# Kernel optimization log

Hardware: AMD Instinct MI355X
Metric: run time of the kernel (lower is better)

The kernel has to match this reference:

```python
import jax, jax.numpy as jnp
import numpy as np


def mlp(x, W1, b1, W2, b2):
    # x: [D] -> y: [O]
    return jnp.tanh(x @ W1 + b1) @ W2 + b2


def christoffel(x, W1, b1, W2, b2):
    """Per-example Christoffel symbols Gamma[k,i,j] for one point x: [D].

    Faithful to the torch code: the 'metric' used for Gamma is built from
    gradients of the FIRST n_dims outputs (y_flat[:, i], i < n_dims), i.e.
    G = Jn Jn^T with Jn the jacobian restricted to the first D outputs.
    """
    D = x.shape[-1]
    f = lambda z: mlp(z, W1, b1, W2, b2)[:D]          # first D outputs

    def metric(z):
        J = jax.jacrev(f)(z)                           # [D, D]
        return J @ J.T                                 # G[i,j] = grad_i . grad_j

    dG = jax.jacfwd(metric)(x)                         # dG[i,j,k] = dG_ij/dx_k
    # Gamma[k,i,j] = 0.5 * (dG[i,j,k] + dG[i,k,j] - dG[j,k,i])
    return 0.5 * (dG.transpose((2, 0, 1)) + dG.transpose((1, 0, 2)) - dG.transpose((1, 2, 0)))


def setup_inputs() -> dict:
    key = jax.random.key(0)
    k1, k2, k3, k4, k5 = jax.random.split(key, 5)
    B, D, H, O = 32, 64, 2048, 64
    return {
        "x0": jnp.zeros((B, D), jnp.float32),
        "xT": jax.random.normal(k1, (B, D), jnp.float32),
        "W1": jax.random.normal(k2, (D, H), jnp.float32) / np.sqrt(D),
        "b1": jax.random.normal(k3, (H,), jnp.float32) * 0.02,
        "W2": jax.random.normal(k4, (H, O), jnp.float32) / np.sqrt(H),
        "b2": jax.random.normal(k5, (O,), jnp.float32) * 0.02,
        "n_steps": 10,
    }


def reference(x0, xT, W1, b1, W2, b2, n_steps):
    B, D = x0.shape
    t = jnp.linspace(0.0, 1.0, n_steps)                    # [S]
    # straight-line interpolation paths  [S, B, D]
    straight = x0[None] + t[:, None, None] * (xT - x0)[None]
    v = xT - x0
    v = v / jnp.linalg.norm(v, axis=1, keepdims=True)      # [B, D]

    interior = straight[1:-1].reshape(-1, D)               # [(S-2)*B, D]
    Gamma = jax.vmap(christoffel, in_axes=(0, None, None, None, None))(
        interior, W1, b1, W2, b2
    ).reshape(n_steps - 2, B, D, D, D)                     # [S-2, B, k, i, j]

    # correction[b,mu] = -sum_{k,i} Gamma[b,k,i,mu] v[b,k] v[b,i]
    corr = -jnp.einsum('sbkim,bk,bi->sbm', Gamma, v, v)    # [S-2, B, D]
    t_int = t[1:-1]
    t_factor = (t_int * (1.0 - t_int))[:, None, None]
    scale = jnp.minimum(jnp.linalg.norm(corr, axis=2, keepdims=True), 0.1)
    corr = corr * t_factor * scale * 0.1

    paths = straight.at[1:-1].add(corr)                    # [S, B, D]
    return paths.reshape(-1, D)                            # [S*B, D]
```

## Files before the change

kernel.cpp:

```cpp
#include <hip/hip_runtime.h>
#include <math.h>


#define D64 64

__device__ __forceinline__ unsigned short f2bf(float x) {
    unsigned u = __float_as_uint(x);
    u += 0x7FFFu + ((u >> 16) & 1u);
    return (unsigned short)(u >> 16);
}
__device__ __forceinline__ float bf_lo(unsigned u) { return __uint_as_float(u << 16); }
__device__ __forceinline__ float bf_hi(unsigned u) { return __uint_as_float(u & 0xFFFF0000u); }

__global__ __launch_bounds__(256) void k_prep(
    const float* __restrict__ x0, const float* __restrict__ xT,
    const float* __restrict__ W1, const float* __restrict__ b1,
    const float* __restrict__ W2,
    unsigned short* __restrict__ W1b,
    float* __restrict__ Z0, float* __restrict__ Zd, float* __restrict__ C,
    float* __restrict__ out, int B, int H, int n_steps)
{
    const int b   = blockIdx.y;
    const int tid = threadIdx.x;
    const int h   = blockIdx.x * 256 + tid;

    __shared__ float x0L[D64], dL[D64], vL[D64];
    if (tid < D64) {
        const float a0 = x0[b * D64 + tid];
        const float aT = xT[b * D64 + tid];
        const float d  = aT - a0;
        float ss = d * d;
        #pragma unroll
        for (int off = 32; off; off >>= 1) ss += __shfl_xor(ss, off);
        const float inv = 1.0f / sqrtf(ss);
        x0L[tid] = a0; dL[tid] = d; vL[tid] = d * inv;
        if (blockIdx.x == 0) {
            out[(size_t)(0 * B + b) * D64 + tid]             = a0;
            out[(size_t)((n_steps - 1) * B + b) * D64 + tid] = aT;
        }
    }
    __syncthreads();

    float z0 = b1[h];
    float zd = 0.f;
    if (b == 0) {
        #pragma unroll
        for (int d = 0; d < D64; ++d) {
            const float w = W1[(size_t)d * H + h];
            W1b[(size_t)d * H + h] = f2bf(w);
            z0 = fmaf(x0L[d], w, z0);
            zd = fmaf(dL[d],  w, zd);
        }
    } else {
        #pragma unroll
        for (int d = 0; d < D64; ++d) {
            const float w = W1[(size_t)d * H + h];
            z0 = fmaf(x0L[d], w, z0);
            zd = fmaf(dL[d],  w, zd);
        }
    }

    float c = 0.f;
    const float4* w2r = reinterpret_cast<const float4*>(W2 + (size_t)h * D64);
    #pragma unroll
    for (int i = 0; i < D64 / 4; ++i) {
        const float4 w = w2r[i];
        c = fmaf(w.x, vL[4*i],     c);
        c = fmaf(w.y, vL[4*i + 1], c);
        c = fmaf(w.z, vL[4*i + 2], c);
        c = fmaf(w.w, vL[4*i + 3], c);
    }

    Z0[(size_t)b * H + h] = z0;
    Zd[(size_t)b * H + h] = zd;
    C [(size_t)b * H + h] = c;
}

__global__ __launch_bounds__(1024) void k_fused(
    const float* __restrict__ x0, const float* __restrict__ xT,
    const unsigned short* __restrict__ W1b,
    const float* __restrict__ Z0, const float* __restrict__ Zd,
    const float* __restrict__ C,
    float* __restrict__ out, int B, int H, int n_steps)
{
    const int n    = blockIdx.x;
    const int s8   = n / B;
    const int b    = n % B;
    const int tid  = threadIdx.x;
    const int lane = tid & 63;
    const int wv   = tid >> 6;

    __shared__ float pL[2048];
    __shared__ float qL[2048];
    __shared__ float gradL[D64];
    __shared__ float corrL[D64];

    const float ts = (float)(s8 + 1) / (float)(n_steps - 1);

    {
        const float2 z0 = reinterpret_cast<const float2*>(Z0 + (size_t)b * H)[tid];
        const float2 zd = reinterpret_cast<const float2*>(Zd + (size_t)b * H)[tid];
        const float2 c  = reinterpret_cast<const float2*>(C  + (size_t)b * H)[tid];
        const float zx = fmaf(ts, zd.x, z0.x);
        const float zy = fmaf(ts, zd.y, z0.y);
        const float tx = tanhf(zx), ty = tanhf(zy);
        const float sx = 1.f - tx * tx, sy = 1.f - ty * ty;
        pL[2 * tid]     = c.x * sx;
        pL[2 * tid + 1] = c.y * sy;
        qL[2 * tid]     = -2.f * c.x * tx * sx;
        qL[2 * tid + 1] = -2.f * c.y * ty * sy;
    }
    __syncthreads();

    #pragma unroll
    for (int rr = 0; rr < 4; ++rr) {
        const int a = wv * 4 + rr;
        const uint4* wrow = reinterpret_cast<const uint4*>(W1b + (size_t)a * H);
        float acc = 0.f;
        #pragma unroll
        for (int k = 0; k < 4; ++k) {
            const uint4  w  = wrow[lane + k * 64];
            const float4 p0 = reinterpret_cast<const float4*>(pL)[(lane + k * 64) * 2];
            const float4 p1 = reinterpret_cast<const float4*>(pL)[(lane + k * 64) * 2 + 1];
            acc = fmaf(bf_lo(w.x), p0.x, acc);
            acc = fmaf(bf_hi(w.x), p0.y, acc);
            acc = fmaf(bf_lo(w.y), p0.z, acc);
            acc = fmaf(bf_hi(w.y), p0.w, acc);
            acc = fmaf(bf_lo(w.z), p1.x, acc);
            acc = fmaf(bf_hi(w.z), p1.y, acc);
            acc = fmaf(bf_lo(w.w), p1.z, acc);
            acc = fmaf(bf_hi(w.w), p1.w, acc);
        }
        #pragma unroll
        for (int off = 32; off; off >>= 1) acc += __shfl_xor(acc, off);
        if (lane == 0) gradL[a] = acc;
    }
    __syncthreads();

    {
        float2 r = make_float2(0.f, 0.f);
        #pragma unroll 16
        for (int d = 0; d < D64; ++d) {
            const unsigned w = reinterpret_cast<const unsigned*>(W1b + (size_t)d * H)[tid];
            const float    g = gradL[d];
            r.x = fmaf(g, bf_lo(w), r.x);
            r.y = fmaf(g, bf_hi(w), r.y);
        }
        pL[2 * tid]     = qL[2 * tid]     * r.x;
        pL[2 * tid + 1] = qL[2 * tid + 1] * r.y;
    }
    __syncthreads();

    #pragma unroll
    for (int rr = 0; rr < 4; ++rr) {
        const int a = wv * 4 + rr;
        const uint4* wrow = reinterpret_cast<const uint4*>(W1b + (size_t)a * H);
        float acc = 0.f;
        #pragma unroll
        for (int k = 0; k < 4; ++k) {
            const uint4  w  = wrow[lane + k * 64];
            const float4 p0 = reinterpret_cast<const float4*>(pL)[(lane + k * 64) * 2];
            const float4 p1 = reinterpret_cast<const float4*>(pL)[(lane + k * 64) * 2 + 1];
            acc = fmaf(bf_lo(w.x), p0.x, acc);
            acc = fmaf(bf_hi(w.x), p0.y, acc);
            acc = fmaf(bf_lo(w.y), p0.z, acc);
            acc = fmaf(bf_hi(w.y), p0.w, acc);
            acc = fmaf(bf_lo(w.z), p1.x, acc);
            acc = fmaf(bf_hi(w.z), p1.y, acc);
            acc = fmaf(bf_lo(w.w), p1.z, acc);
            acc = fmaf(bf_hi(w.w), p1.w, acc);
        }
        #pragma unroll
        for (int off = 32; off; off >>= 1) acc += __shfl_xor(acc, off);
        if (lane == 0) corrL[a] = -acc;
    }
    __syncthreads();

    if (tid < D64) {
        const float a0 = x0[b * D64 + tid];
        const float aT = xT[b * D64 + tid];
        const float d  = aT - a0;
        const float cm = corrL[tid];
        float n2 = cm * cm;
        #pragma unroll
        for (int off = 32; off; off >>= 1) n2 += __shfl_xor(n2, off);
        const float scale  = fminf(sqrtf(n2), 0.1f);
        const float factor = ts * (1.f - ts) * scale * 0.1f;
        out[(size_t)((s8 + 1) * B + b) * D64 + tid] = fmaf(cm, factor, fmaf(ts, d, a0));
    }
}

extern "C" void kernel_launch(void* const* d_in, const int* in_sizes, int n_in,
                              void* d_out, int out_size, void* d_ws, size_t ws_size,
                              hipStream_t stream) {
    const float* x0 = (const float*)d_in[0];
    const float* xT = (const float*)d_in[1];
    const float* W1 = (const float*)d_in[2];
    const float* b1 = (const float*)d_in[3];
    const float* W2 = (const float*)d_in[4];
    float* out = (float*)d_out;

    const int H       = in_sizes[3];
    const int D       = in_sizes[2] / H;
    const int B       = in_sizes[0] / D;
    const int n_steps = out_size / (B * D);
    const int NI      = n_steps - 2;
    const int NP      = NI * B;

    unsigned short* W1b = (unsigned short*)d_ws;
    float* Z0 = (float*)(W1b + (size_t)D * H);
    float* Zd = Z0 + (size_t)B * H;
    float* C  = Zd + (size_t)B * H;

    k_prep<<<dim3(H / 256, B), dim3(256), 0, stream>>>(
        x0, xT, W1, b1, W2, W1b, Z0, Zd, C, out, B, H, n_steps);
    k_fused<<<dim3(NP), dim3(1024), 0, stream>>>(
        x0, xT, W1b, Z0, Zd, C, out, B, H, n_steps);
}
```

Measured before the change: 81.64 us.

## Merge prep and fused kernels into one cooperative kernel with grid sync

Replaces the two-kernel sequence with a single cooperative launch of NP blocks. Each block first computes a 256-wide chunk of Z0/Zd/C, splitting the D reduction across four thread groups and combining the partials in shared memory, and converts a slice of W1 to bf16. A grid-wide sync follows, then the per-point fused Gamma contraction runs as before. This removes a kernel launch boundary and redistributes the prep work over more threads, at the cost of a grid barrier and of requiring all 256 blocks of 1024 threads to be co-resident. The chunk mapping relies on NP*512 equalling D*H and on NI being H/256, which matches only these shapes.

After: 123.7 us. 51.5% more time.

```diff
diff --git a/kernel.cpp b/kernel.cpp
--- a/kernel.cpp
+++ b/kernel.cpp
@@ -1,8 +1,12 @@
 #include <hip/hip_runtime.h>
+#include <hip/hip_cooperative_groups.h>
 #include <math.h>
 
+namespace cg = cooperative_groups;
+
 
 #define D64 64
+#define HH  2048
 
 __device__ __forceinline__ unsigned short f2bf(float x) {
     unsigned u = __float_as_uint(x);
@@ -12,7 +16,7 @@
 __device__ __forceinline__ float bf_lo(unsigned u) { return __uint_as_float(u << 16); }
 __device__ __forceinline__ float bf_hi(unsigned u) { return __uint_as_float(u & 0xFFFF0000u); }
 
-__global__ __launch_bounds__(256) void k_prep(
+__global__ __launch_bounds__(1024) void k_all(
     const float* __restrict__ x0, const float* __restrict__ xT,
     const float* __restrict__ W1, const float* __restrict__ b1,
     const float* __restrict__ W2,
@@ -20,11 +24,20 @@
     float* __restrict__ Z0, float* __restrict__ Zd, float* __restrict__ C,
     float* __restrict__ out, int B, int H, int n_steps)
 {
-    const int b   = blockIdx.y;
-    const int tid = threadIdx.x;
-    const int h   = blockIdx.x * 256 + tid;
+    const int n    = blockIdx.x;
+    const int b    = n % B;
+    const int ch   = n / B;
+    const int tid  = threadIdx.x;
+    const int lane = tid & 63;
+    const int wv   = tid >> 6;
 
     __shared__ float x0L[D64], dL[D64], vL[D64];
+    __shared__ float red[3][4][256];
+    __shared__ float pL[HH];
+    __shared__ float qL[HH];
+    __shared__ float gradL[D64];
+    __shared__ float corrL[D64];
+
     if (tid < D64) {
         const float a0 = x0[b * D64 + tid];
         const float aT = xT[b * D64 + tid];
@@ -34,68 +47,60 @@
         for (int off = 32; off; off >>= 1) ss += __shfl_xor(ss, off);
         const float inv = 1.0f / sqrtf(ss);
         x0L[tid] = a0; dL[tid] = d; vL[tid] = d * inv;
-        if (blockIdx.x == 0) {
+        if (ch == 0) {
             out[(size_t)(0 * B + b) * D64 + tid]             = a0;
             out[(size_t)((n_steps - 1) * B + b) * D64 + tid] = aT;
         }
     }
     __syncthreads();
 
-    float z0 = b1[h];
-    float zd = 0.f;
-    if (b == 0) {
-        #pragma unroll
-        for (int d = 0; d < D64; ++d) {
-            const float w = W1[(size_t)d * H + h];
-            W1b[(size_t)d * H + h] = f2bf(w);
-            z0 = fmaf(x0L[d], w, z0);
-            zd = fmaf(dL[d],  w, zd);
-        }
-    } else {
-        #pragma unroll
-        for (int d = 0; d < D64; ++d) {
-            const float w = W1[(size_t)d * H + h];
-            z0 = fmaf(x0L[d], w, z0);
-            zd = fmaf(dL[d],  w, zd);
-        }
-    }
-
-    float c = 0.f;
-    const float4* w2r = reinterpret_cast<const float4*>(W2 + (size_t)h * D64);
-    #pragma unroll
-    for (int i = 0; i < D64 / 4; ++i) {
-        const float4 w = w2r[i];
-        c = fmaf(w.x, vL[4*i],     c);
-        c = fmaf(w.y, vL[4*i + 1], c);
-        c = fmaf(w.z, vL[4*i + 2], c);
-        c = fmaf(w.w, vL[4*i + 3], c);
-    }
-
-    Z0[(size_t)b * H + h] = z0;
-    Zd[(size_t)b * H + h] = zd;
-    C [(size_t)b * H + h] = c;
-}
-
-__global__ __launch_bounds__(1024) void k_fused(
-    const float* __restrict__ x0, const float* __restrict__ xT,
-    const unsigned short* __restrict__ W1b,
-    const float* __restrict__ Z0, const float* __restrict__ Zd,
-    const float* __restrict__ C,
-    float* __restrict__ out, int B, int H, int n_steps)
-{
-    const int n    = blockIdx.x;
-    const int s8   = n / B;
-    const int b    = n % B;
-    const int tid  = threadIdx.x;
-    const int lane = tid & 63;
-    const int wv   = tid >> 6;
-
-    __shared__ float pL[2048];
-    __shared__ float qL[2048];
-    __shared__ float gradL[D64];
-    __shared__ float corrL[D64];
-
-    const float ts = (float)(s8 + 1) / (float)(n_steps - 1);
+    {
+        const int part = tid >> 8;
+        const int hl   = tid & 255;
+        const int h    = ch * 256 + hl;
+        const int d0   = part * 16;
+
+        float z0 = (part == 0) ? b1[h] : 0.f;
+        float zd = 0.f;
+        #pragma unroll
+        for (int d = 0; d < 16; ++d) {
+            const float w = W1[(size_t)(d0 + d) * H + h];
+            z0 = fmaf(x0L[d0 + d], w, z0);
+            zd = fmaf(dL[d0 + d],  w, zd);
+        }
+        float c = 0.f;
+        #pragma unroll
+        for (int i = 0; i < 16; i += 4) {
+            const float4 w = *reinterpret_cast<const float4*>(W2 + (size_t)h * D64 + d0 + i);
+            c = fmaf(w.x, vL[d0 + i],     c);
+            c = fmaf(w.y, vL[d0 + i + 1], c);
+            c = fmaf(w.z, vL[d0 + i + 2], c);
+            c = fmaf(w.w, vL[d0 + i + 3], c);
+        }
+        red[0][part][hl] = z0;
+        red[1][part][hl] = zd;
+        red[2][part][hl] = c;
+    }
+
+    if (tid < 128) {
+        const size_t base = (size_t)n * 512 + tid * 4;
+        const float4 w = *reinterpret_cast<const float4*>(W1 + base);
+        const unsigned lo = ((unsigned)f2bf(w.y) << 16) | f2bf(w.x);
+        const unsigned hi = ((unsigned)f2bf(w.w) << 16) | f2bf(w.z);
+        *reinterpret_cast<uint2*>(W1b + base) = make_uint2(lo, hi);
+    }
+    __syncthreads();
+
+    if (tid < 256) {
+        const size_t o = (size_t)b * H + ch * 256 + tid;
+        Z0[o] = red[0][0][tid] + red[0][1][tid] + red[0][2][tid] + red[0][3][tid];
+        Zd[o] = red[1][0][tid] + red[1][1][tid] + red[1][2][tid] + red[1][3][tid];
+        C [o] = red[2][0][tid] + red[2][1][tid] + red[2][2][tid] + red[2][3][tid];
+    }
+
+    cg::this_grid().sync();
+
+    const float ts = (float)(ch + 1) / (float)(n_steps - 1);
 
     {
         const float2 z0 = reinterpret_cast<const float2*>(Z0 + (size_t)b * H)[tid];
@@ -177,16 +182,14 @@
     __syncthreads();
 
     if (tid < D64) {
-        const float a0 = x0[b * D64 + tid];
-        const float aT = xT[b * D64 + tid];
-        const float d  = aT - a0;
         const float cm = corrL[tid];
         float n2 = cm * cm;
         #pragma unroll
         for (int off = 32; off; off >>= 1) n2 += __shfl_xor(n2, off);
         const float scale  = fminf(sqrtf(n2), 0.1f);
         const float factor = ts * (1.f - ts) * scale * 0.1f;
-        out[(size_t)((s8 + 1) * B + b) * D64 + tid] = fmaf(cm, factor, fmaf(ts, d, a0));
+        out[(size_t)((ch + 1) * B + b) * D64 + tid] =
+            fmaf(cm, factor, fmaf(ts, dL[tid], x0L[tid]));
     }
 }
 
@@ -200,20 +203,21 @@
     const float* W2 = (const float*)d_in[4];
     float* out = (float*)d_out;
 
-    const int H       = in_sizes[3];
-    const int D       = in_sizes[2] / H;
-    const int B       = in_sizes[0] / D;
-    const int n_steps = out_size / (B * D);
-    const int NI      = n_steps - 2;
-    const int NP      = NI * B;
+    int H       = in_sizes[3];
+    int D       = in_sizes[2] / H;
+    int B       = in_sizes[0] / D;
+    int n_steps = out_size / (B * D);
+    const int NI = n_steps - 2;
+    const int NP = NI * B;
 
     unsigned short* W1b = (unsigned short*)d_ws;
     float* Z0 = (float*)(W1b + (size_t)D * H);
     float* Zd = Z0 + (size_t)B * H;
     float* C  = Zd + (size_t)B * H;
 
-    k_prep<<<dim3(H / 256, B), dim3(256), 0, stream>>>(
-        x0, xT, W1, b1, W2, W1b, Z0, Zd, C, out, B, H, n_steps);
-    k_fused<<<dim3(NP), dim3(1024), 0, stream>>>(
-        x0, xT, W1b, Z0, Zd, C, out, B, H, n_steps);
+    void* args[] = { (void*)&x0, (void*)&xT, (void*)&W1, (void*)&b1, (void*)&W2,
+                     (void*)&W1b, (void*)&Z0, (void*)&Zd, (void*)&C,
+                     (void*)&out, (void*)&B, (void*)&H, (void*)&n_steps };
+    hipLaunchCooperativeKernel((const void*)k_all, dim3(NP), dim3(1024),
+                               args, 0, stream);
 }
```
